# Performance work log

Measured on AMD Instinct MI355X. Metric: run time of the kernel, lower is better.

Reference implementation:

```python
import jax, jax.numpy as jnp
import numpy as np

B, CIN, H, W = 32, 1, 512, 512
PATCH = 16
PW, PH = H // PATCH, W // PATCH  # 32, 32
S = PW * PH                      # 1024 tokens
C = 256
L = 8
POOL = 4
OUT_IDX = (2, 4, 6)
EPS = 1e-5


def setup_inputs() -> dict:
    key = jax.random.key(0)
    ks = jax.random.split(key, 10)
    sc = 1.0 / np.sqrt(C).astype(np.float32)
    return {
        "image": jax.random.normal(ks[0], (B, CIN, H, W), jnp.float32),
        "conv_w": jax.random.normal(ks[1], (C, CIN), jnp.float32),
        "conv_b": jnp.zeros((C,), jnp.float32),
        "feat_w": jax.random.normal(ks[2], (C, C), jnp.float32) * sc,
        "feat_b": jnp.zeros((C,), jnp.float32),
        "ln_s": jnp.ones((L, C), jnp.float32),
        "ln_b": jnp.zeros((L, C), jnp.float32),
        "wq": jax.random.normal(ks[3], (L, C, C), jnp.float32) * sc,
        "bq": jnp.zeros((L, C), jnp.float32),
        "wk": jax.random.normal(ks[4], (L, C, C), jnp.float32) * sc,
        "bk": jnp.zeros((L, C), jnp.float32),
        "wv": jax.random.normal(ks[5], (L, C, C), jnp.float32) * sc,
        "bv": jnp.zeros((L, C), jnp.float32),
        "wf": jax.random.normal(ks[6], (L, C, C), jnp.float32) * sc,
        "bf": jnp.zeros((L, C), jnp.float32),
        "wa": jax.random.normal(ks[7], (L, C, 2 * C), jnp.float32) * sc,
        "ba": jnp.zeros((L, 2 * C), jnp.float32),
    }


def _to_spatial(t):  # [B,S,C] -> [B,C,PW,PH]
    return t.transpose(0, 2, 1).reshape(t.shape[0], C, PW, PH)


def _to_seq(t):  # [B,C,PW,PH] -> [B,S,C]
    return t.reshape(t.shape[0], C, S).transpose(0, 2, 1)


def _layernorm(x, s, b):
    mu = x.mean(-1, keepdims=True)
    var = x.var(-1, keepdims=True)
    return (x - mu) * jax.lax.rsqrt(var + EPS) * s + b


def _attention(x, Wq, bq, Wk, bk, Wv, bv):
    d = np.float32(1.0 / np.sqrt(C))
    Q = _to_spatial(jax.nn.sigmoid(x @ Wq + bq))
    K = _to_spatial(jax.nn.sigmoid(x @ Wk + bk))
    V = _to_spatial(jax.nn.sigmoid(x @ Wv + bv))
    # avg_pool2d with kernel (POOL, 1): pool rows of the patch grid
    qp = Q.reshape(B, C, PW // POOL, POOL, PH).mean(3)
    kp = K.reshape(B, C, PW // POOL, POOL, PH).mean(3)
    # dual softmax low-rank factorization, per channel
    Qk = jax.nn.softmax(d * jnp.einsum('ncik,ncjk->ncij', Q, kp), axis=-1)   # [B,C,PW,PW/POOL]
    Kq = jax.nn.softmax(d * jnp.einsum('ncik,ncjk->ncij', qp, K), axis=-1)   # [B,C,PW/POOL,PW]
    Kqv = jnp.einsum('ncik,nckj->ncij', Kq, V)                               # [B,C,PW/POOL,PH]
    return _to_seq(jnp.einsum('ncik,nckj->ncij', Qk, Kqv))                   # [B,S,C]


def _forward(image, conv_w, conv_b, feat_w, feat_b, ln_s, ln_b,
             wq, bq, wk, bk, wv, bv, wf, bf, wa, ba):
    # Conv2d(kernel=1, stride=patch) == strided subsample + 1x1 projection
    xs = image[:, :, ::PATCH, ::PATCH]                                       # [B,1,PW,PH]
    emb = jnp.einsum('bihw,oi->bohw', xs, conv_w) + conv_b[None, :, None, None]
    x = jnp.tanh(_to_seq(emb) @ feat_w + feat_b)                             # [B,S,C]
    hid, att = [], []
    for l in range(L):
        tn = _layernorm(x, ln_s[l], ln_b[l])
        a = _attention(tn, wq[l], bq[l], wk[l], bk[l], wv[l], bv[l])
        ta = x + a
        # FiLM adaptive norm: sigmoid linear -> interleaved (scale, shift) pairs
        sh = jax.nn.sigmoid(ta @ wa[l] + ba[l]).reshape(B, S, C, 2)
        tn2 = sh[..., 0] * ta + sh[..., 1]
        x = jax.nn.relu(tn2 @ wf[l] + bf[l]) + ta
        if l in OUT_IDX:
            hid.append(x)
            att.append(ta)
    # pack: [last; 3 intermediate hiddens; 3 attention residuals] -> [7,B,S,C]
    return jnp.concatenate([x[None], jnp.stack(hid), jnp.stack(att)], axis=0)


def reference(image, conv_w, conv_b, feat_w, feat_b, ln_s, ln_b,
              wq, bq, wk, bk, wv, bv, wf, bf, wa, ba):
    return _forward(image, conv_w, conv_b, feat_w, feat_b, ln_s, ln_b,
                    wq, bq, wk, bk, wv, bv, wf, bf, wa, ba)
```

## Files before the change

### kernel.cpp

```cpp
#include <hip/hip_runtime.h>
#include <hip/hip_bf16.h>
#include <cstdint>
#include <cstddef>

#define B_ 32
#define C_ 256
#define S_ 1024
#define L_ 8

typedef unsigned short bf16_t;
typedef __attribute__((ext_vector_type(8))) short s8v;
typedef __attribute__((ext_vector_type(4))) short s4v;
typedef __attribute__((ext_vector_type(4))) float f4v;

static __device__ __forceinline__ float b2f(bf16_t v) {
    unsigned int u = ((unsigned int)v) << 16;
    float f;
    __builtin_memcpy(&f, &u, 4);
    return f;
}
static __device__ __forceinline__ bf16_t f2b(float f) {
    unsigned int u;
    __builtin_memcpy(&u, &f, 4);
    u += 0x7fffu + ((u >> 16) & 1u);
    return (bf16_t)(u >> 16);
}
static __device__ __forceinline__ float sigmoidf_(float x) {
    return 1.0f / (1.0f + __expf(-x));
}
static __device__ __forceinline__ void gload_lds16(const void* g, void* l) {
    __builtin_amdgcn_global_load_lds((const __attribute__((address_space(1))) void*)g,
                                     (__attribute__((address_space(3))) void*)l, 16, 0, 0);
}


__global__ void make_xs_k(const float* __restrict__ img, float* __restrict__ xs) {
    int t = blockIdx.x * 256 + threadIdx.x;
    if (t >= B_ * S_) return;
    int b = t >> 10, s = t & 1023, i = s >> 5, k = s & 31;
    xs[t] = img[(size_t)b * 512 * 512 + (size_t)(i * 16) * 512 + k * 16];
}

__global__ void fuse_wb_k(const float* __restrict__ cw, const float* __restrict__ cb,
                          const float* __restrict__ fwm, const float* __restrict__ fbv,
                          float* __restrict__ fw, float* __restrict__ fb) {
    int c = threadIdx.x;
    float a = 0.f, bs = 0.f;
    for (int o = 0; o < C_; o++) {
        float f = fwm[o * C_ + c];
        a += cw[o] * f;
        bs += cb[o] * f;
    }
    fw[c] = a;
    fb[c] = bs + fbv[c];
}

__global__ __launch_bounds__(256) void wtrans_k(const float* __restrict__ wq, const float* __restrict__ wk,
                                                const float* __restrict__ wv, const float* __restrict__ wf,
                                                const float* __restrict__ wa, const float* __restrict__ ln_s,
                                                bf16_t* __restrict__ WT) {
    __shared__ float t[32][33];
    int z = blockIdx.z, l = z / 6, tp = z - l * 6;
    const float* src;
    int ld, cmul, coff;
    if (tp < 4) {
        const float* bases[4] = {wq, wk, wv, wf};
        src = bases[tp] + (size_t)l * 65536;
        ld = 256; cmul = 1; coff = 0;
    } else {
        src = wa + (size_t)l * 131072;
        ld = 512; cmul = 2; coff = tp - 4;
    }
    const float* g = ln_s + l * 256;
    bf16_t* dst = WT + ((size_t)l * 6 + tp) * 65536;
    int k0 = blockIdx.y * 32, m0 = blockIdx.x * 32;
    int tx = threadIdx.x & 31, ty = threadIdx.x >> 5;
#pragma unroll
    for (int r = 0; r < 4; ++r) {
        int k = k0 + ty + 8 * r;
        float v = src[(size_t)k * ld + (m0 + tx) * cmul + coff];
        if (tp < 3) v *= g[k];
        t[ty + 8 * r][tx] = v;
    }
    __syncthreads();
#pragma unroll
    for (int r = 0; r < 4; ++r)
        dst[(size_t)(m0 + ty + 8 * r) * 256 + k0 + tx] = f2b(t[tx][ty + 8 * r]);
}

__global__ __launch_bounds__(256) void colsum_k(const bf16_t* __restrict__ WT,
                                                const float* __restrict__ wq, const float* __restrict__ wk,
                                                const float* __restrict__ wv,
                                                const float* __restrict__ bq, const float* __restrict__ bk,
                                                const float* __restrict__ bv,
                                                const float* __restrict__ ln_b,
                                                float* __restrict__ csum, float* __restrict__ bias2) {
    int m = threadIdx.x, mat = blockIdx.x, l = blockIdx.y;
    const bf16_t* wt = WT + ((size_t)l * 6 + mat) * 65536 + (size_t)m * 256;
    float cs = 0.f;
    for (int k = 0; k < 256; k += 8) {
        s8v u = *(const s8v*)(wt + k);
#pragma unroll
        for (int j = 0; j < 8; ++j) cs += b2f((bf16_t)u[j]);
    }
    const float* worig = (mat == 0 ? wq : mat == 1 ? wk : wv) + (size_t)l * 65536;
    const float* borig = (mat == 0 ? bq : mat == 1 ? bk : bv) + l * 256;
    const float* lb = ln_b + l * 256;
    float bb = 0.f;
    for (int k = 0; k < 256; ++k) bb += lb[k] * worig[(size_t)k * 256 + m];
    int o = (l * 3 + mat) * 256 + m;
    csum[o] = cs;
    bias2[o] = bb + borig[m];
}

__global__ __launch_bounds__(256) void embed_k(const float* __restrict__ xs, const float* __restrict__ fw,
                                               const float* __restrict__ fb, bf16_t* __restrict__ X) {
    int wid = threadIdx.x >> 6, lane = threadIdx.x & 63;
    int row = blockIdx.x * 4 + wid;
    float xv = xs[row];
    f4v fwv = *(const f4v*)(fw + lane * 4);
    f4v fbv = *(const f4v*)(fb + lane * 4);
    s4v o;
#pragma unroll
    for (int j = 0; j < 4; ++j) o[j] = (short)f2b(tanhf(xv * fwv[j] + fbv[j]));
    *(s4v*)(X + (size_t)row * 256 + lane * 4) = o;
}

__global__ __launch_bounds__(256) void stats_k(const bf16_t* __restrict__ X,
                                               float* __restrict__ rs, float* __restrict__ rsmu) {
    int wid = threadIdx.x >> 6, lane = threadIdx.x & 63;
    int row = blockIdx.x * 4 + wid;
    s4v v = *(const s4v*)(X + (size_t)row * 256 + lane * 4);
    float sum = 0.f, sq = 0.f;
#pragma unroll
    for (int j = 0; j < 4; ++j) {
        float f = b2f((bf16_t)v[j]);
        sum += f;
        sq += f * f;
    }
#pragma unroll
    for (int off = 32; off > 0; off >>= 1) {
        sum += __shfl_xor(sum, off);
        sq += __shfl_xor(sq, off);
    }
    if (lane == 0) {
        float mu = sum * (1.f / 256.f);
        float var = sq * (1.f / 256.f) - mu * mu;
        float r = rsqrtf(var + 1e-5f);
        rs[row] = r;
        rsmu[row] = r * mu;
    }
}

template <int MODE, bool HID>
__global__ __launch_bounds__(256) void mm_k(const bf16_t* Ain,
                                            const bf16_t* __restrict__ W0,
                                            const bf16_t* __restrict__ W1,
                                            const float* __restrict__ bias0,
                                            const float* __restrict__ csP,
                                            const float* __restrict__ rs,
                                            const float* __restrict__ rsmu,
                                            const bf16_t* ta,
                                            bf16_t* O0, bf16_t* O1, bf16_t* O2,
                                            float* __restrict__ hid) {
    __shared__ char lds[32768];
    char* XS = lds;
    char* WS0 = lds + 16384;
    char* WS1 = lds + 24576;
    const int tid = threadIdx.x, lane = tid & 63, wid = tid >> 6;
    const int wrow = wid >> 1, wcol = wid & 1;
    const int s0 = blockIdx.y * 128, mt0 = blockIdx.x * 64, b = blockIdx.z;

    const int lr8 = lane >> 3;
    const int cb0 = ((lane & 7) << 4) ^ (lr8 << 4);

    const char* Ag = (const char*)Ain + (((size_t)b * 1024 + s0) * 256) * 2 + cb0;
    const char* Wg0 = (const char*)W0 + ((size_t)mt0 * 256) * 2 + cb0;
    const char* Wg1 = (const char*)W1 + ((size_t)mt0 * 256) * 2 + cb0;

    f4v acc[4][2] = {};
    f4v acc1[4][2] = {};

    for (int kt = 0; kt < 4; ++kt) {
        const char* ga = Ag + kt * 128;
#pragma unroll
        for (int q = 0; q < 4; ++q) {
            int r0 = wid * 32 + q * 8;
            gload_lds16(ga + (size_t)(r0 + lr8) * 512, XS + r0 * 128);
        }
        const char* gw = Wg0 + kt * 128;
#pragma unroll
        for (int p = 0; p < 2; ++p) {
            int r0 = wid * 16 + p * 8;
            gload_lds16(gw + (size_t)(r0 + lr8) * 512, WS0 + r0 * 128);
        }
        if constexpr (MODE == 1) {
            const char* gw1 = Wg1 + kt * 128;
#pragma unroll
            for (int p = 0; p < 2; ++p) {
                int r0 = wid * 16 + p * 8;
                gload_lds16(gw1 + (size_t)(r0 + lr8) * 512, WS1 + r0 * 128);
            }
        }
        __syncthreads();
#pragma unroll
        for (int kk = 0; kk < 2; ++kk) {
            const int cb = kk * 64 + ((lane >> 4) << 4);
            s8v av[4];
#pragma unroll
            for (int mi = 0; mi < 4; ++mi) {
                int r = wrow * 64 + mi * 16 + (lane & 15);
                av[mi] = *(const s8v*)(XS + r * 128 + (cb ^ ((r & 7) << 4)));
            }
            s8v bv[2], bw[2];
#pragma unroll
            for (int ni = 0; ni < 2; ++ni) {
                int m = wcol * 32 + ni * 16 + (lane & 15);
                bv[ni] = *(const s8v*)(WS0 + m * 128 + (cb ^ ((m & 7) << 4)));
                if constexpr (MODE == 1)
                    bw[ni] = *(const s8v*)(WS1 + m * 128 + (cb ^ ((m & 7) << 4)));
            }
#pragma unroll
            for (int mi = 0; mi < 4; ++mi)
#pragma unroll
                for (int ni = 0; ni < 2; ++ni) {
                    acc[mi][ni] = __builtin_amdgcn_mfma_f32_16x16x32_bf16(av[mi], bv[ni], acc[mi][ni], 0, 0, 0);
                    if constexpr (MODE == 1)
                        acc1[mi][ni] = __builtin_amdgcn_mfma_f32_16x16x32_bf16(av[mi], bw[ni], acc1[mi][ni], 0, 0, 0);
                }
        }
        __syncthreads();
    }

    if constexpr (MODE == 0) {
        const int mat = mt0 >> 8, mw = mt0 & 255;
        const float* bs = bias0 + mat * 256 + mw;
        const float* cs = csP + mat * 256 + mw;
        bf16_t* Os = (mat == 0) ? O0 : (mat == 1 ? O1 : O2);
        bf16_t* T = (bf16_t*)lds;
#pragma unroll
        for (int mi = 0; mi < 4; ++mi)
#pragma unroll
            for (int r = 0; r < 4; ++r) {
                int sl = wrow * 64 + mi * 16 + (lane >> 4) * 4 + r;
                int sg = b * 1024 + s0 + sl;
                float a = rs[sg], cc = rsmu[sg];
#pragma unroll
                for (int ni = 0; ni < 2; ++ni) {
                    int ml = wcol * 32 + ni * 16 + (lane & 15);
                    float v = sigmoidf_(a * acc[mi][ni][r] - cc * cs[ml] + bs[ml]);
                    T[ml * 144 + sl] = f2b(v);
                }
            }
        __syncthreads();
        int m = tid >> 2, c0s = (tid & 3) * 32;
        bf16_t* dst = Os + ((size_t)(b * 256 + mw + m)) * 1024 + s0 + c0s;
#pragma unroll
        for (int j = 0; j < 4; ++j)
            *(s8v*)(dst + j * 8) = *(const s8v*)(T + m * 144 + c0s + j * 8);
    } else {
#pragma unroll
        for (int mi = 0; mi < 4; ++mi)
#pragma unroll
            for (int ni = 0; ni < 2; ++ni) {
                int ml = mt0 + wcol * 32 + ni * 16 + (lane & 15);
#pragma unroll
                for (int r = 0; r < 4; ++r) {
                    int sg = b * 1024 + s0 + wrow * 64 + mi * 16 + (lane >> 4) * 4 + r;
                    size_t idx = (size_t)sg * 256 + ml;
                    if constexpr (MODE == 1) {
                        float v = sigmoidf_(acc[mi][ni][r] + bias0[2 * ml]) * b2f(ta[idx]) +
                                  sigmoidf_(acc1[mi][ni][r] + bias0[2 * ml + 1]);
                        O0[idx] = f2b(v);
                    } else {
                        float v = fmaxf(acc[mi][ni][r] + bias0[ml], 0.f) + b2f(ta[idx]);
                        O0[idx] = f2b(v);
                        if constexpr (HID) hid[idx] = v;
                    }
                }
            }
    }
}

__global__ __launch_bounds__(256) void attn_k(const bf16_t* __restrict__ Q, const bf16_t* __restrict__ K,
                                              const bf16_t* __restrict__ V, bf16_t* __restrict__ A) {
    __shared__ char Lds[40960];
    const int w = threadIdx.x >> 6, lane = threadIdx.x & 63;
    char* P = Lds + w * 10240;
    const int gw = blockIdx.x * 4 + w;
    const int b = gw >> 8, c = gw & 255;
    const size_t base = ((size_t)b * 256 + c) * 1024;
    constexpr int QO = 0, KO = 2560, VTO = 5120, QPO = 7680, KPO = 8960;
    const f4v zf = {0.f, 0.f, 0.f, 0.f};

    {
        const s8v* Qg = (const s8v*)(Q + base);
        const s8v* Kg = (const s8v*)(K + base);
        const s8v* Vg = (const s8v*)(V + base);
        s8v q0 = Qg[lane * 2], q1 = Qg[lane * 2 + 1];
        s8v k0 = Kg[lane * 2], k1 = Kg[lane * 2 + 1];
        s8v v0 = Vg[lane * 2], v1 = Vg[lane * 2 + 1];
        int rowoff = (lane >> 1) * 80 + (lane & 1) * 32;
        *(s8v*)(P + QO + rowoff) = q0;
        *(s8v*)(P + QO + rowoff + 16) = q1;
        *(s8v*)(P + KO + rowoff) = k0;
        *(s8v*)(P + KO + rowoff + 16) = k1;
        int pw = lane >> 1, ph0 = (lane & 1) * 16;
#pragma unroll
        for (int j = 0; j < 8; ++j) {
            *(bf16_t*)(P + VTO + (ph0 + j) * 80 + pw * 2) = (bf16_t)(unsigned short)v0[j];
            *(bf16_t*)(P + VTO + (ph0 + 8 + j) * 80 + pw * 2) = (bf16_t)(unsigned short)v1[j];
        }
    }
    __syncthreads();
#pragma unroll
    for (int e = 0; e < 2; ++e) {
        int idx = lane + 64 * e;
        int i2 = idx >> 4, kp2 = idx & 15;
        float q0 = 0.f, q1 = 0.f, k0 = 0.f, k1 = 0.f;
#pragma unroll
        for (int p = 0; p < 4; ++p) {
            unsigned int uq = *(const unsigned int*)(P + QO + (4 * i2 + p) * 80 + kp2 * 4);
            unsigned int uk = *(const unsigned int*)(P + KO + (4 * i2 + p) * 80 + kp2 * 4);
            q0 += b2f((bf16_t)(uq & 0xffff)); q1 += b2f((bf16_t)(uq >> 16));
            k0 += b2f((bf16_t)(uk & 0xffff)); k1 += b2f((bf16_t)(uk >> 16));
        }
        *(unsigned int*)(P + QPO + i2 * 80 + kp2 * 4) =
            (unsigned int)f2b(q0 * 0.25f) | ((unsigned int)f2b(q1 * 0.25f) << 16);
        *(unsigned int*)(P + KPO + i2 * 80 + kp2 * 4) =
            (unsigned int)f2b(k0 * 0.25f) | ((unsigned int)f2b(k1 * 0.25f) << 16);
    }
    __syncthreads();
    const int frow = lane & 15, fcol = (lane >> 4) * 16;
    s8v aq0 = *(const s8v*)(P + QO + frow * 80 + fcol);
    s8v aq1 = *(const s8v*)(P + QO + (16 + frow) * 80 + fcol);
    s8v bkp = *(const s8v*)(P + KPO + frow * 80 + fcol);
    s8v aqp = *(const s8v*)(P + QPO + frow * 80 + fcol);
    s8v bk0 = *(const s8v*)(P + KO + frow * 80 + fcol);
    s8v bk1 = *(const s8v*)(P + KO + (16 + frow) * 80 + fcol);
    f4v s1a = __builtin_amdgcn_mfma_f32_16x16x32_bf16(aq0, bkp, zf, 0, 0, 0);
    f4v s1b = __builtin_amdgcn_mfma_f32_16x16x32_bf16(aq1, bkp, zf, 0, 0, 0);
    f4v s2a = __builtin_amdgcn_mfma_f32_16x16x32_bf16(aqp, bk0, zf, 0, 0, 0);
    f4v s2b = __builtin_amdgcn_mfma_f32_16x16x32_bf16(aqp, bk1, zf, 0, 0, 0);
    __syncthreads();
    {
        int zr = lane & 31, zh = (lane >> 5) * 16;
        *(f4v*)(P + QO + zr * 80 + 16 + zh) = zf;
        *(f4v*)(P + QO + zr * 80 + 48 + zh) = zf;
        *(f4v*)(P + KO + zr * 80 + 16 + zh) = zf;
        *(f4v*)(P + KO + zr * 80 + 48 + zh) = zf;
    }
    const float dsc = 0.0625f;
    {
        int j = lane & 15;
#pragma unroll
        for (int t = 0; t < 2; ++t) {
            f4v av = t ? s1b : s1a;
#pragma unroll
            for (int r = 0; r < 4; ++r) {
                float x = av[r] * dsc;
                float m = x;
                m = fmaxf(m, __shfl_xor(m, 1));
                m = fmaxf(m, __shfl_xor(m, 2));
                m = fmaxf(m, __shfl_xor(m, 4));
                float e2 = __expf(x - m);
                float s = e2;
                s += __shfl_xor(s, 1);
                s += __shfl_xor(s, 2);
                s += __shfl_xor(s, 4);
                float p = e2 / s;
                if (j < 8) {
                    int row = t * 16 + (lane >> 4) * 4 + r;
                    *(bf16_t*)(P + QO + row * 80 + j * 2) = f2b(p);
                }
            }
        }
    }
#pragma unroll
    for (int r = 0; r < 4; ++r) {
        float xa = s2a[r] * dsc, xb = s2b[r] * dsc;
        float m = fmaxf(xa, xb);
        m = fmaxf(m, __shfl_xor(m, 1));
        m = fmaxf(m, __shfl_xor(m, 2));
        m = fmaxf(m, __shfl_xor(m, 4));
        m = fmaxf(m, __shfl_xor(m, 8));
        float ea = __expf(xa - m), eb = __expf(xb - m);
        float s = ea + eb;
        s += __shfl_xor(s, 1);
        s += __shfl_xor(s, 2);
        s += __shfl_xor(s, 4);
        s += __shfl_xor(s, 8);
        float inv = 1.f / s;
        if (lane < 32) {
            int row = (lane >> 4) * 4 + r;
            *(bf16_t*)(P + QPO + row * 80 + frow * 2) = f2b(ea * inv);
            *(bf16_t*)(P + QPO + row * 80 + (16 + frow) * 2) = f2b(eb * inv);
        }
    }
    __syncthreads();
    {
        s8v as2 = *(const s8v*)(P + QPO + frow * 80 + fcol);
        s8v bv0 = *(const s8v*)(P + VTO + frow * 80 + fcol);
        s8v bv1 = *(const s8v*)(P + VTO + (16 + frow) * 80 + fcol);
        f4v k3a = __builtin_amdgcn_mfma_f32_16x16x32_bf16(as2, bv0, zf, 0, 0, 0);
        f4v k3b = __builtin_amdgcn_mfma_f32_16x16x32_bf16(as2, bv1, zf, 0, 0, 0);
        if (lane < 32) {
#pragma unroll
            for (int r = 0; r < 4; ++r) {
                int jj = (lane >> 4) * 4 + r;
                *(bf16_t*)(P + KO + frow * 80 + jj * 2) = f2b(k3a[r]);
                *(bf16_t*)(P + KO + (16 + frow) * 80 + jj * 2) = f2b(k3b[r]);
            }
        }
    }
    __syncthreads();
    {
        s8v a40 = *(const s8v*)(P + QO + frow * 80 + fcol);
        s8v a41 = *(const s8v*)(P + QO + (16 + frow) * 80 + fcol);
        s8v b40 = *(const s8v*)(P + KO + frow * 80 + fcol);
        s8v b41 = *(const s8v*)(P + KO + (16 + frow) * 80 + fcol);
        f4v o00 = __builtin_amdgcn_mfma_f32_16x16x32_bf16(a40, b40, zf, 0, 0, 0);
        f4v o01 = __builtin_amdgcn_mfma_f32_16x16x32_bf16(a40, b41, zf, 0, 0, 0);
        f4v o10 = __builtin_amdgcn_mfma_f32_16x16x32_bf16(a41, b40, zf, 0, 0, 0);
        f4v o11 = __builtin_amdgcn_mfma_f32_16x16x32_bf16(a41, b41, zf, 0, 0, 0);
#pragma unroll
        for (int r = 0; r < 4; ++r) {
            int r0 = (lane >> 4) * 4 + r;
            *(bf16_t*)(P + VTO + r0 * 80 + frow * 2) = f2b(o00[r]);
            *(bf16_t*)(P + VTO + r0 * 80 + (16 + frow) * 2) = f2b(o01[r]);
            *(bf16_t*)(P + VTO + (16 + r0) * 80 + frow * 2) = f2b(o10[r]);
            *(bf16_t*)(P + VTO + (16 + r0) * 80 + (16 + frow) * 2) = f2b(o11[r]);
        }
    }
    __syncthreads();
    {
        int i = lane >> 1, hh = (lane & 1) * 32;
        s8v r0 = *(const s8v*)(P + VTO + i * 80 + hh);
        s8v r1 = *(const s8v*)(P + VTO + i * 80 + hh + 16);
        *(s8v*)(A + base + lane * 16) = r0;
        *(s8v*)(A + base + lane * 16 + 8) = r1;
    }
}

template <bool SNAP>
__global__ __launch_bounds__(256) void add_tr_k(const bf16_t* __restrict__ Aa, bf16_t* X,
                                                float* __restrict__ att) {
    __shared__ float T[32][33];
    int b = blockIdx.z, c0 = blockIdx.y * 32, s0 = blockIdx.x * 32;
    int tx = threadIdx.x & 31, ty = threadIdx.x >> 5;
#pragma unroll
    for (int r = 0; r < 4; ++r)
        T[ty + 8 * r][tx] = b2f(Aa[((size_t)(b * 256 + c0 + ty + 8 * r)) * 1024 + s0 + tx]);
    __syncthreads();
#pragma unroll
    for (int r = 0; r < 4; ++r) {
        int s = s0 + ty + 8 * r;
        size_t idx = ((size_t)(b * 1024 + s)) * 256 + c0 + tx;
        float v = b2f(X[idx]) + T[tx][ty + 8 * r];
        X[idx] = f2b(v);
        if constexpr (SNAP) att[idx] = v;
    }
}


extern "C" void kernel_launch(void* const* d_in, const int* in_sizes, int n_in,
                              void* d_out, int out_size, void* d_ws, size_t ws_size,
                              hipStream_t stream) {
    const float* image  = (const float*)d_in[0];
    const float* conv_w = (const float*)d_in[1];
    const float* conv_b = (const float*)d_in[2];
    const float* feat_w = (const float*)d_in[3];
    const float* feat_b = (const float*)d_in[4];
    const float* ln_s   = (const float*)d_in[5];
    const float* ln_b   = (const float*)d_in[6];
    const float* wq     = (const float*)d_in[7];
    const float* bq     = (const float*)d_in[8];
    const float* wk     = (const float*)d_in[9];
    const float* bk     = (const float*)d_in[10];
    const float* wv     = (const float*)d_in[11];
    const float* bv     = (const float*)d_in[12];
    const float* wf     = (const float*)d_in[13];
    const float* bfv    = (const float*)d_in[14];
    const float* wa     = (const float*)d_in[15];
    const float* ba     = (const float*)d_in[16];
    float* out = (float*)d_out;

    char* p = (char*)d_ws;
    const size_t MB16 = (size_t)B_ * S_ * C_ * sizeof(bf16_t);
    float* xs    = (float*)p;  p += 131072;
    float* fw    = (float*)p;  p += 1024;
    float* fb    = (float*)p;  p += 1024;
    float* rsb   = (float*)p;  p += 131072;
    float* rsmub = (float*)p;  p += 131072;
    float* csum  = (float*)p;  p += 24576;
    float* bias2 = (float*)p;  p += 24576;
    bf16_t* WT = (bf16_t*)p;   p += (size_t)48 * 65536 * 2;
    bf16_t* X  = (bf16_t*)p;   p += MB16;
    bf16_t* T1 = (bf16_t*)p;   p += MB16;
    bf16_t* T2 = (bf16_t*)p;   p += MB16;
    bf16_t* Qb = (bf16_t*)p;   p += MB16;
    bf16_t* Kb = (bf16_t*)p;   p += MB16;
    bf16_t* Vb = (bf16_t*)p;   p += MB16;
    size_t needed = (size_t)(p - (char*)d_ws);
    if (ws_size < needed) Vb = (bf16_t*)d_out;

    make_xs_k<<<128, 256, 0, stream>>>(image, xs);
    fuse_wb_k<<<1, 256, 0, stream>>>(conv_w, conv_b, feat_w, feat_b, fw, fb);
    wtrans_k<<<dim3(8, 8, 48), 256, 0, stream>>>(wq, wk, wv, wf, wa, ln_s, WT);
    colsum_k<<<dim3(3, 8), 256, 0, stream>>>(WT, wq, wk, wv, bq, bk, bv, ln_b, csum, bias2);
    embed_k<<<8192, 256, 0, stream>>>(xs, fw, fb, X);

    const size_t slot = (size_t)B_ * S_ * C_;

    for (int l = 0; l < L_; ++l) {
        const bf16_t* WTl = WT + (size_t)l * 6 * 65536;
        int snap = (l == 2) ? 0 : (l == 4) ? 1 : (l == 6) ? 2 : -1;

        stats_k<<<8192, 256, 0, stream>>>(X, rsb, rsmub);
        mm_k<0, false><<<dim3(12, 8, 32), 256, 0, stream>>>(
            X, WTl, nullptr, bias2 + l * 768, csum + l * 768, rsb, rsmub, nullptr, Qb, Kb, Vb, nullptr);
        attn_k<<<2048, 256, 0, stream>>>(Qb, Kb, Vb, T1);
        if (snap >= 0)
            add_tr_k<true><<<dim3(32, 8, 32), 256, 0, stream>>>(T1, X, out + (size_t)(4 + snap) * slot);
        else
            add_tr_k<false><<<dim3(32, 8, 32), 256, 0, stream>>>(T1, X, nullptr);
        mm_k<1, false><<<dim3(4, 8, 32), 256, 0, stream>>>(
            X, WTl + 4 * 65536, WTl + 5 * 65536, ba + l * 512, nullptr, nullptr, nullptr, X, T2, nullptr, nullptr, nullptr);
        float* hid = (snap >= 0) ? out + (size_t)(1 + snap) * slot : (l == 7 ? out : nullptr);
        if (hid)
            mm_k<2, true><<<dim3(4, 8, 32), 256, 0, stream>>>(
                T2, WTl + 3 * 65536, nullptr, bfv + l * 256, nullptr, nullptr, nullptr, X, X, nullptr, nullptr, hid);
        else
            mm_k<2, false><<<dim3(4, 8, 32), 256, 0, stream>>>(
                T2, WTl + 3 * 65536, nullptr, bfv + l * 256, nullptr, nullptr, nullptr, X, X, nullptr, nullptr, nullptr);
    }
}
```

Measured before the change: 1.158 ms.

## Drop block barriers in attention, fuse first LN stats into embed, widen stats

The attention kernel now loads Q/K fragments and computes the row pooling straight from global memory into registers. It keeps only the transposed V and softmax scratch in a smaller per-wave LDS region, and replaces block-wide __syncthreads with wave barriers, since each wave works on its own channel. The layer-0 LayerNorm statistics are computed inside embed_k, and stats_k processes two rows per wave with half the blocks. The LDS footprint of mm_k mode 0 grows slightly, which may change occupancy.

```diff
diff --git a/kernel.cpp b/kernel.cpp
--- a/kernel.cpp
+++ b/kernel.cpp
@@ -114,36 +114,57 @@
 }
 
 __global__ __launch_bounds__(256) void embed_k(const float* __restrict__ xs, const float* __restrict__ fw,
-                                               const float* __restrict__ fb, bf16_t* __restrict__ X) {
+                                               const float* __restrict__ fb, bf16_t* __restrict__ X,
+                                               float* __restrict__ rs, float* __restrict__ rsmu) {
     int wid = threadIdx.x >> 6, lane = threadIdx.x & 63;
     int row = blockIdx.x * 4 + wid;
     float xv = xs[row];
     f4v fwv = *(const f4v*)(fw + lane * 4);
     f4v fbv = *(const f4v*)(fb + lane * 4);
     s4v o;
-#pragma unroll
-    for (int j = 0; j < 4; ++j) o[j] = (short)f2b(tanhf(xv * fwv[j] + fbv[j]));
+    float sum = 0.f, sq = 0.f;
+#pragma unroll
+    for (int j = 0; j < 4; ++j) {
+        float v = tanhf(xv * fwv[j] + fbv[j]);
+        float vb = b2f(f2b(v));
+        o[j] = (short)f2b(v);
+        sum += vb;
+        sq += vb * vb;
+    }
     *(s4v*)(X + (size_t)row * 256 + lane * 4) = o;
+#pragma unroll
+    for (int off = 32; off > 0; off >>= 1) {
+        sum += __shfl_xor(sum, off);
+        sq += __shfl_xor(sq, off);
+    }
+    if (lane == 0) {
+        float mu = sum * (1.f / 256.f);
+        float var = sq * (1.f / 256.f) - mu * mu;
+        float r = rsqrtf(var + 1e-5f);
+        rs[row] = r;
+        rsmu[row] = r * mu;
+    }
 }
 
 __global__ __launch_bounds__(256) void stats_k(const bf16_t* __restrict__ X,
                                                float* __restrict__ rs, float* __restrict__ rsmu) {
     int wid = threadIdx.x >> 6, lane = threadIdx.x & 63;
-    int row = blockIdx.x * 4 + wid;
-    s4v v = *(const s4v*)(X + (size_t)row * 256 + lane * 4);
+    int row2 = blockIdx.x * 8 + wid * 2;
+    s8v v = *(const s8v*)(X + (size_t)row2 * 256 + lane * 8);
     float sum = 0.f, sq = 0.f;
 #pragma unroll
-    for (int j = 0; j < 4; ++j) {
+    for (int j = 0; j < 8; ++j) {
         float f = b2f((bf16_t)v[j]);
         sum += f;
         sq += f * f;
     }
 #pragma unroll
-    for (int off = 32; off > 0; off >>= 1) {
+    for (int off = 16; off > 0; off >>= 1) {
         sum += __shfl_xor(sum, off);
         sq += __shfl_xor(sq, off);
     }
-    if (lane == 0) {
+    if ((lane & 31) == 0) {
+        int row = row2 + (lane >> 5);
         float mu = sum * (1.f / 256.f);
         float var = sq * (1.f / 256.f) - mu * mu;
         float r = rsqrtf(var + 1e-5f);
@@ -163,7 +184,8 @@
                                             const bf16_t* ta,
                                             bf16_t* O0, bf16_t* O1, bf16_t* O2,
                                             float* __restrict__ hid) {
-    __shared__ char lds[32768];
+    constexpr int LDSZ = (MODE == 0) ? 34816 : 32768;
+    __shared__ char lds[LDSZ];
     char* XS = lds;
     char* WS0 = lds + 16384;
     char* WS1 = lds + 24576;
@@ -284,72 +306,70 @@
 
 __global__ __launch_bounds__(256) void attn_k(const bf16_t* __restrict__ Q, const bf16_t* __restrict__ K,
                                               const bf16_t* __restrict__ V, bf16_t* __restrict__ A) {
-    __shared__ char Lds[40960];
+    __shared__ char Lds[35840];
     const int w = threadIdx.x >> 6, lane = threadIdx.x & 63;
-    char* P = Lds + w * 10240;
+    char* P = Lds + w * 8960;
     const int gw = blockIdx.x * 4 + w;
     const int b = gw >> 8, c = gw & 255;
     const size_t base = ((size_t)b * 256 + c) * 1024;
-    constexpr int QO = 0, KO = 2560, VTO = 5120, QPO = 7680, KPO = 8960;
+    constexpr int VT = 0, S1 = 2560, S2 = 5120, KQ = 6400;
     const f4v zf = {0.f, 0.f, 0.f, 0.f};
-
+    const int frow = lane & 15, fhalf = lane >> 4;
+    const int fbyte = fhalf * 16;
+    const bf16_t* Qg = Q + base;
+    const bf16_t* Kg = K + base;
+    const bf16_t* Vg = V + base;
+
+    s8v aq0 = *(const s8v*)(Qg + frow * 32 + fhalf * 8);
+    s8v aq1 = *(const s8v*)(Qg + (16 + frow) * 32 + fhalf * 8);
+    s8v bk0 = *(const s8v*)(Kg + frow * 32 + fhalf * 8);
+    s8v bk1 = *(const s8v*)(Kg + (16 + frow) * 32 + fhalf * 8);
+    float accq[8], acck[8];
+#pragma unroll
+    for (int j = 0; j < 8; ++j) { accq[j] = 0.f; acck[j] = 0.f; }
+#pragma unroll
+    for (int pp = 0; pp < 4; ++pp) {
+        int rr = 4 * frow + pp;
+        if (rr > 31) rr = 31;
+        s8v uq = *(const s8v*)(Qg + rr * 32 + fhalf * 8);
+        s8v uk = *(const s8v*)(Kg + rr * 32 + fhalf * 8);
+#pragma unroll
+        for (int j = 0; j < 8; ++j) {
+            accq[j] += b2f((bf16_t)uq[j]);
+            acck[j] += b2f((bf16_t)uk[j]);
+        }
+    }
+    s8v aqp, bkp;
+#pragma unroll
+    for (int j = 0; j < 8; ++j) {
+        aqp[j] = (short)f2b(accq[j] * 0.25f);
+        bkp[j] = (short)f2b(acck[j] * 0.25f);
+    }
     {
-        const s8v* Qg = (const s8v*)(Q + base);
-        const s8v* Kg = (const s8v*)(K + base);
-        const s8v* Vg = (const s8v*)(V + base);
-        s8v q0 = Qg[lane * 2], q1 = Qg[lane * 2 + 1];
-        s8v k0 = Kg[lane * 2], k1 = Kg[lane * 2 + 1];
-        s8v v0 = Vg[lane * 2], v1 = Vg[lane * 2 + 1];
-        int rowoff = (lane >> 1) * 80 + (lane & 1) * 32;
-        *(s8v*)(P + QO + rowoff) = q0;
-        *(s8v*)(P + QO + rowoff + 16) = q1;
-        *(s8v*)(P + KO + rowoff) = k0;
-        *(s8v*)(P + KO + rowoff + 16) = k1;
+        s8v v0 = *(const s8v*)(Vg + lane * 16);
+        s8v v1 = *(const s8v*)(Vg + lane * 16 + 8);
         int pw = lane >> 1, ph0 = (lane & 1) * 16;
 #pragma unroll
         for (int j = 0; j < 8; ++j) {
-            *(bf16_t*)(P + VTO + (ph0 + j) * 80 + pw * 2) = (bf16_t)(unsigned short)v0[j];
-            *(bf16_t*)(P + VTO + (ph0 + 8 + j) * 80 + pw * 2) = (bf16_t)(unsigned short)v1[j];
-        }
-    }
-    __syncthreads();
-#pragma unroll
-    for (int e = 0; e < 2; ++e) {
-        int idx = lane + 64 * e;
-        int i2 = idx >> 4, kp2 = idx & 15;
-        float q0 = 0.f, q1 = 0.f, k0 = 0.f, k1 = 0.f;
-#pragma unroll
-        for (int p = 0; p < 4; ++p) {
-            unsigned int uq = *(const unsigned int*)(P + QO + (4 * i2 + p) * 80 + kp2 * 4);
-            unsigned int uk = *(const unsigned int*)(P + KO + (4 * i2 + p) * 80 + kp2 * 4);
-            q0 += b2f((bf16_t)(uq & 0xffff)); q1 += b2f((bf16_t)(uq >> 16));
-            k0 += b2f((bf16_t)(uk & 0xffff)); k1 += b2f((bf16_t)(uk >> 16));
-        }
-        *(unsigned int*)(P + QPO + i2 * 80 + kp2 * 4) =
-            (unsigned int)f2b(q0 * 0.25f) | ((unsigned int)f2b(q1 * 0.25f) << 16);
-        *(unsigned int*)(P + KPO + i2 * 80 + kp2 * 4) =
-            (unsigned int)f2b(k0 * 0.25f) | ((unsigned int)f2b(k1 * 0.25f) << 16);
-    }
-    __syncthreads();
-    const int frow = lane & 15, fcol = (lane >> 4) * 16;
-    s8v aq0 = *(const s8v*)(P + QO + frow * 80 + fcol);
-    s8v aq1 = *(const s8v*)(P + QO + (16 + frow) * 80 + fcol);
-    s8v bkp = *(const s8v*)(P + KPO + frow * 80 + fcol);
-    s8v aqp = *(const s8v*)(P + QPO + frow * 80 + fcol);
-    s8v bk0 = *(const s8v*)(P + KO + frow * 80 + fcol);
-    s8v bk1 = *(const s8v*)(P + KO + (16 + frow) * 80 + fcol);
+            *(bf16_t*)(P + VT + (ph0 + j) * 80 + pw * 2) = (bf16_t)(unsigned short)v0[j];
+            *(bf16_t*)(P + VT + (ph0 + 8 + j) * 80 + pw * 2) = (bf16_t)(unsigned short)v1[j];
+        }
+    }
+    if (lane < 32) {
+#pragma unroll
+        for (int q = 0; q < 4; ++q) *(f4v*)(P + S1 + lane * 80 + q * 16) = zf;
+#pragma unroll
+        for (int q = 0; q < 3; ++q) *(f4v*)(P + KQ + lane * 80 + 16 + q * 16) = zf;
+    } else if (lane < 40) {
+#pragma unroll
+        for (int q = 0; q < 4; ++q) *(f4v*)(P + S2 + (lane - 24) * 80 + q * 16) = zf;
+    }
+
     f4v s1a = __builtin_amdgcn_mfma_f32_16x16x32_bf16(aq0, bkp, zf, 0, 0, 0);
     f4v s1b = __builtin_amdgcn_mfma_f32_16x16x32_bf16(aq1, bkp, zf, 0, 0, 0);
     f4v s2a = __builtin_amdgcn_mfma_f32_16x16x32_bf16(aqp, bk0, zf, 0, 0, 0);
     f4v s2b = __builtin_amdgcn_mfma_f32_16x16x32_bf16(aqp, bk1, zf, 0, 0, 0);
-    __syncthreads();
-    {
-        int zr = lane & 31, zh = (lane >> 5) * 16;
-        *(f4v*)(P + QO + zr * 80 + 16 + zh) = zf;
-        *(f4v*)(P + QO + zr * 80 + 48 + zh) = zf;
-        *(f4v*)(P + KO + zr * 80 + 16 + zh) = zf;
-        *(f4v*)(P + KO + zr * 80 + 48 + zh) = zf;
-    }
+
     const float dsc = 0.0625f;
     {
         int j = lane & 15;
@@ -370,8 +390,8 @@
                 s += __shfl_xor(s, 4);
                 float p = e2 / s;
                 if (j < 8) {
-                    int row = t * 16 + (lane >> 4) * 4 + r;
-                    *(bf16_t*)(P + QO + row * 80 + j * 2) = f2b(p);
+                    int row = t * 16 + fhalf * 4 + r;
+                    *(bf16_t*)(P + S1 + row * 80 + j * 2) = f2b(p);
                 }
             }
         }
@@ -392,51 +412,51 @@
         s += __shfl_xor(s, 8);
         float inv = 1.f / s;
         if (lane < 32) {
-            int row = (lane >> 4) * 4 + r;
-            *(bf16_t*)(P + QPO + row * 80 + frow * 2) = f2b(ea * inv);
-            *(bf16_t*)(P + QPO + row * 80 + (16 + frow) * 2) = f2b(eb * inv);
-        }
-    }
-    __syncthreads();
+            int row = fhalf * 4 + r;
+            *(bf16_t*)(P + S2 + row * 80 + frow * 2) = f2b(ea * inv);
+            *(bf16_t*)(P + S2 + row * 80 + (16 + frow) * 2) = f2b(eb * inv);
+        }
+    }
+    __builtin_amdgcn_wave_barrier();
     {
-        s8v as2 = *(const s8v*)(P + QPO + frow * 80 + fcol);
-        s8v bv0 = *(const s8v*)(P + VTO + frow * 80 + fcol);
-        s8v bv1 = *(const s8v*)(P + VTO + (16 + frow) * 80 + fcol);
+        s8v as2 = *(const s8v*)(P + S2 + frow * 80 + fbyte);
+        s8v bv0 = *(const s8v*)(P + VT + frow * 80 + fbyte);
+        s8v bv1 = *(const s8v*)(P + VT + (16 + frow) * 80 + fbyte);
         f4v k3a = __builtin_amdgcn_mfma_f32_16x16x32_bf16(as2, bv0, zf, 0, 0, 0);
         f4v k3b = __builtin_amdgcn_mfma_f32_16x16x32_bf16(as2, bv1, zf, 0, 0, 0);
         if (lane < 32) {
 #pragma unroll
             for (int r = 0; r < 4; ++r) {
-                int jj = (lane >> 4) * 4 + r;
-                *(bf16_t*)(P + KO + frow * 80 + jj * 2) = f2b(k3a[r]);
-                *(bf16_t*)(P + KO + (16 + frow) * 80 + jj * 2) = f2b(k3b[r]);
-            }
-        }
-    }
-    __syncthreads();
+                int i2 = fhalf * 4 + r;
+                *(bf16_t*)(P + KQ + frow * 80 + i2 * 2) = f2b(k3a[r]);
+                *(bf16_t*)(P + KQ + (16 + frow) * 80 + i2 * 2) = f2b(k3b[r]);
+            }
+        }
+    }
+    __builtin_amdgcn_wave_barrier();
     {
-        s8v a40 = *(const s8v*)(P + QO + frow * 80 + fcol);
-        s8v a41 = *(const s8v*)(P + QO + (16 + frow) * 80 + fcol);
-        s8v b40 = *(const s8v*)(P + KO + frow * 80 + fcol);
-        s8v b41 = *(const s8v*)(P + KO + (16 + frow) * 80 + fcol);
+        s8v a40 = *(const s8v*)(P + S1 + frow * 80 + fbyte);
+        s8v a41 = *(const s8v*)(P + S1 + (16 + frow) * 80 + fbyte);
+        s8v b40 = *(const s8v*)(P + KQ + frow * 80 + fbyte);
+        s8v b41 = *(const s8v*)(P + KQ + (16 + frow) * 80 + fbyte);
         f4v o00 = __builtin_amdgcn_mfma_f32_16x16x32_bf16(a40, b40, zf, 0, 0, 0);
         f4v o01 = __builtin_amdgcn_mfma_f32_16x16x32_bf16(a40, b41, zf, 0, 0, 0);
         f4v o10 = __builtin_amdgcn_mfma_f32_16x16x32_bf16(a41, b40, zf, 0, 0, 0);
         f4v o11 = __builtin_amdgcn_mfma_f32_16x16x32_bf16(a41, b41, zf, 0, 0, 0);
 #pragma unroll
         for (int r = 0; r < 4; ++r) {
-            int r0 = (lane >> 4) * 4 + r;
-            *(bf16_t*)(P + VTO + r0 * 80 + frow * 2) = f2b(o00[r]);
-            *(bf16_t*)(P + VTO + r0 * 80 + (16 + frow) * 2) = f2b(o01[r]);
-            *(bf16_t*)(P + VTO + (16 + r0) * 80 + frow * 2) = f2b(o10[r]);
-            *(bf16_t*)(P + VTO + (16 + r0) * 80 + (16 + frow) * 2) = f2b(o11[r]);
-        }
-    }
-    __syncthreads();
+            int r0 = fhalf * 4 + r;
+            *(bf16_t*)(P + VT + r0 * 80 + frow * 2) = f2b(o00[r]);
+            *(bf16_t*)(P + VT + r0 * 80 + (16 + frow) * 2) = f2b(o01[r]);
+            *(bf16_t*)(P + VT + (16 + r0) * 80 + frow * 2) = f2b(o10[r]);
+            *(bf16_t*)(P + VT + (16 + r0) * 80 + (16 + frow) * 2) = f2b(o11[r]);
+        }
+    }
+    __builtin_amdgcn_wave_barrier();
     {
         int i = lane >> 1, hh = (lane & 1) * 32;
-        s8v r0 = *(const s8v*)(P + VTO + i * 80 + hh);
-        s8v r1 = *(const s8v*)(P + VTO + i * 80 + hh + 16);
+        s8v r0 = *(const s8v*)(P + VT + i * 80 + hh);
+        s8v r1 = *(const s8v*)(P + VT + i * 80 + hh + 16);
         *(s8v*)(A + base + lane * 16) = r0;
         *(s8v*)(A + base + lane * 16 + 8) = r1;
     }
@@ -508,7 +528,7 @@
     fuse_wb_k<<<1, 256, 0, stream>>>(conv_w, conv_b, feat_w, feat_b, fw, fb);
     wtrans_k<<<dim3(8, 8, 48), 256, 0, stream>>>(wq, wk, wv, wf, wa, ln_s, WT);
     colsum_k<<<dim3(3, 8), 256, 0, stream>>>(WT, wq, wk, wv, bq, bk, bv, ln_b, csum, bias2);
-    embed_k<<<8192, 256, 0, stream>>>(xs, fw, fb, X);
+    embed_k<<<8192, 256, 0, stream>>>(xs, fw, fb, X, rsb, rsmub);
 
     const size_t slot = (size_t)B_ * S_ * C_;
 
@@ -516,7 +536,7 @@
         const bf16_t* WTl = WT + (size_t)l * 6 * 65536;
         int snap = (l == 2) ? 0 : (l == 4) ? 1 : (l == 6) ? 2 : -1;
 
-        stats_k<<<8192, 256, 0, stream>>>(X, rsb, rsmub);
+        if (l > 0) stats_k<<<4096, 256, 0, stream>>>(X, rsb, rsmub);
         mm_k<0, false><<<dim3(12, 8, 32), 256, 0, stream>>>(
             X, WTl, nullptr, bias2 + l * 768, csum + l * 768, rsb, rsmub, nullptr, Qb, Kb, Vb, nullptr);
         attn_k<<<2048, 256, 0, stream>>>(Qb, Kb, Vb, T1);
```

Measured after the change: 1.140 ms. No clear change (-1.5%).
